# Kernel tuning notes

Measured on AMD Instinct MI355X. Metric: run time of the kernel, lower is better.

## Reference

```python
import jax, jax.numpy as jnp
import numpy as np

BATCH, SEQ, DIM, NH = 4, 2048, 1024, 16
HD = DIM // NH  # 64

def _rope_cos_sin(seq_len, head_dim, dtype=jnp.float32):
    inv_freq = 1.0 / (10000.0 ** (jnp.arange(0, head_dim, 2, dtype=dtype) / head_dim))
    t = jnp.arange(seq_len, dtype=dtype)
    freqs = jnp.outer(t, inv_freq)                # (seq, hd/2)
    emb = jnp.concatenate([freqs, freqs], axis=-1)  # (seq, hd)
    return jnp.cos(emb), jnp.sin(emb)

def _apply_rope(x, cos, sin):
    # x: (b, h, s, d); cos/sin: (s, d)
    d2 = x.shape[-1] // 2
    x1, x2 = x[..., :d2], x[..., d2:]
    c = cos[None, None, :, :d2]
    s = sin[None, None, :, :d2]
    return jnp.concatenate([x1 * c - x2 * s, x1 * s + x2 * c], axis=-1)

def setup_inputs() -> dict:
    key = jax.random.key(0)
    ks = jax.random.split(key, 3)
    x = jax.random.normal(ks[0], (BATCH, SEQ, DIM), dtype=jnp.float32)
    Wqkv = jax.random.normal(ks[1], (DIM, 3 * DIM), dtype=jnp.float32) * (1.0 / np.sqrt(DIM))
    bqkv = jnp.zeros((3 * DIM,), dtype=jnp.float32)
    Wout = jax.random.normal(ks[2], (DIM, DIM), dtype=jnp.float32) * (1.0 / np.sqrt(DIM))
    bout = jnp.zeros((DIM,), dtype=jnp.float32)
    return {"x": x, "Wqkv": Wqkv, "bqkv": bqkv, "Wout": Wout, "bout": bout}

def reference(x, Wqkv, bqkv, Wout, bout):
    b, s, dim = x.shape
    qkv = x @ Wqkv + bqkv                          # (b, s, 3*dim)
    qkv = qkv.reshape(b, s, 3, NH, HD).transpose(2, 0, 3, 1, 4)  # (3, b, h, s, hd)
    q, k, v = qkv[0], qkv[1], qkv[2]
    cos, sin = _rope_cos_sin(s, HD, x.dtype)
    q = _apply_rope(q, cos, sin)
    k = _apply_rope(k, cos, sin)
    scale = HD ** -0.5
    scores = jnp.einsum('bhqd,bhkd->bhqk', q, k) * scale
    attn = jax.nn.softmax(scores, axis=-1)
    attn = jnp.nan_to_num(attn, nan=0.0)
    out = jnp.einsum('bhqk,bhkd->bhqd', attn, v)   # (b, h, s, hd)
    out = out.transpose(0, 2, 1, 3).reshape(b, s, dim)
    return out @ Wout + bout
```

## Files before the change

### kernel.cpp

```cpp
#include <hip/hip_runtime.h>
#include <hip/hip_bf16.h>
#include <stdint.h>

#define DEVI __device__ __forceinline__

typedef __attribute__((ext_vector_type(8))) short bf16x8;
typedef __attribute__((ext_vector_type(4))) float f32x4;

DEVI float bf2f(short u) {
  union { unsigned int i; float f; } v;
  v.i = ((unsigned int)(unsigned short)u) << 16;
  return v.f;
}
DEVI short f2bf(float f) {
  union { float f; unsigned int i; } v; v.f = f;
  unsigned int r = v.i + 0x7FFFu + ((v.i >> 16) & 1u);
  return (short)(r >> 16);
}

DEVI bf16x8 ldsfrag(const short* t, int row, int k0) {
  int slot = k0 >> 3;
  return *(const bf16x8*)(t + row * 64 + ((slot ^ (row & 7)) << 3));
}

DEVI void gload16(const void* g, void* l) {
  __builtin_amdgcn_global_load_lds((const __attribute__((address_space(1))) void*)g,
                                   (__attribute__((address_space(3))) void*)l, 16, 0, 0);
}

__global__ void k_cvt(const float* __restrict__ in, short* __restrict__ out, int n4) {
  int i = blockIdx.x * blockDim.x + threadIdx.x;
  if (i >= n4) return;
  float4 v = ((const float4*)in)[i];
  short4 o;
  o.x = f2bf(v.x); o.y = f2bf(v.y); o.z = f2bf(v.z); o.w = f2bf(v.w);
  ((short4*)out)[i] = o;
}

__global__ void k_transpose_bf16(const float* __restrict__ in, short* __restrict__ outp,
                                 int R, int C) {
  __shared__ float tile[32][33];
  const int c0 = blockIdx.x * 32, r0 = blockIdx.y * 32;
  const int tx = threadIdx.x, ty = threadIdx.y;
  for (int i = ty; i < 32; i += 8) tile[i][tx] = in[(size_t)(r0 + i) * C + c0 + tx];
  __syncthreads();
  for (int i = ty; i < 32; i += 8) outp[(size_t)(c0 + i) * R + r0 + tx] = f2bf(tile[tx][i]);
}

__global__ void k_rope(float* __restrict__ cosT, float* __restrict__ sinT) {
  int idx = blockIdx.x * blockDim.x + threadIdx.x;
  int s = idx >> 5, i = idx & 31;
  float inv = exp2f(-0.41524101186092034f * (float)i);
  float freq = (float)s * inv;
  cosT[idx] = cosf(freq);
  sinT[idx] = sinf(freq);
}

template <int OUTF32>
__global__ __launch_bounds__(256) void k_gemm(const short* __restrict__ A,
                                              const short* __restrict__ BT,
                                              const float* __restrict__ bias,
                                              void* __restrict__ outp,
                                              int M, int N, int K) {
  __shared__ __align__(16) short As[128 * 64];
  __shared__ __align__(16) short Bs[128 * 64];
  const int tid = threadIdx.x;
  const int lane = tid & 63, wid = tid >> 6;
  const int ln = lane & 15, grp = lane >> 4;
  const int wm = wid >> 1, wn = wid & 1;
  const int r0 = blockIdx.y * 128, c0 = blockIdx.x * 128;

  const short* aSrc[4];
  const short* bSrc[4];
  int ldst[4];
#pragma unroll
  for (int j = 0; j < 4; ++j) {
    int chunk = wid * 256 + j * 64 + lane;
    int row = chunk >> 3, gs = (chunk & 7) ^ (row & 7);
    aSrc[j] = A + (size_t)(r0 + row) * K + gs * 8;
    bSrc[j] = BT + (size_t)(c0 + row) * K + gs * 8;
    ldst[j] = (wid * 256 + j * 64) * 8;
  }

  f32x4 acc[4][4];
#pragma unroll
  for (int i = 0; i < 4; ++i)
#pragma unroll
    for (int j = 0; j < 4; ++j) acc[i][j] = (f32x4){0.f, 0.f, 0.f, 0.f};

  const int nkt = K >> 6;
  for (int kt = 0; kt < nkt; ++kt) {
    __syncthreads();
#pragma unroll
    for (int j = 0; j < 4; ++j) {
      gload16(aSrc[j], &As[ldst[j]]);
      gload16(bSrc[j], &Bs[ldst[j]]);
      aSrc[j] += 64;
      bSrc[j] += 64;
    }
    __syncthreads();
#pragma unroll
    for (int ks = 0; ks < 2; ++ks) {
      const int k0 = ks * 32 + grp * 8;
      bf16x8 af[4], bfr[4];
#pragma unroll
      for (int mi = 0; mi < 4; ++mi) af[mi] = ldsfrag(As, wm * 64 + mi * 16 + ln, k0);
#pragma unroll
      for (int ni = 0; ni < 4; ++ni) bfr[ni] = ldsfrag(Bs, wn * 64 + ni * 16 + ln, k0);
#pragma unroll
      for (int mi = 0; mi < 4; ++mi)
#pragma unroll
        for (int ni = 0; ni < 4; ++ni)
          acc[mi][ni] = __builtin_amdgcn_mfma_f32_16x16x32_bf16(af[mi], bfr[ni], acc[mi][ni], 0, 0, 0);
    }
  }
#pragma unroll
  for (int ni = 0; ni < 4; ++ni) {
    const int col = c0 + wn * 64 + ni * 16 + ln;
    const float bv = bias[col];
#pragma unroll
    for (int mi = 0; mi < 4; ++mi) {
#pragma unroll
      for (int r = 0; r < 4; ++r) {
        const int rowg = r0 + wm * 64 + mi * 16 + grp * 4 + r;
        float v = acc[mi][ni][r] + bv;
        if (OUTF32) ((float*)outp)[(size_t)rowg * N + col] = v;
        else        ((short*)outp)[(size_t)rowg * N + col] = f2bf(v);
      }
    }
  }
}

__global__ __launch_bounds__(256) void k_transform(const short* __restrict__ qkv,
                                                   const float* __restrict__ cosT,
                                                   const float* __restrict__ sinT,
                                                   short* __restrict__ qo,
                                                   short* __restrict__ ko,
                                                   short* __restrict__ vp) {
  __shared__ __align__(16) short vs[64 * 72];
  const int st = blockIdx.x, bh = blockIdx.y;
  const int b = bh >> 4, h = bh & 15;
  const int t = threadIdx.x;
  const float QSC = 0.18033688011112042f;
  {
    const int sl = t >> 2, j = t & 3;
    const int s = st * 64 + sl;
    const short* row = qkv + ((size_t)(b * 2048 + s)) * 3072 + h * 64;
    bf16x8 qlo = *(const bf16x8*)(row + j * 8);
    bf16x8 qhi = *(const bf16x8*)(row + 32 + j * 8);
    bf16x8 klo = *(const bf16x8*)(row + 1024 + j * 8);
    bf16x8 khi = *(const bf16x8*)(row + 1056 + j * 8);
    const float* cp = cosT + s * 32 + j * 8;
    const float* sp = sinT + s * 32 + j * 8;
    bf16x8 ql, qh, kl, kh;
#pragma unroll
    for (int e = 0; e < 8; ++e) {
      float c = cp[e], sn = sp[e];
      float a1 = bf2f(qlo[e]), a2 = bf2f(qhi[e]);
      ql[e] = f2bf((a1 * c - a2 * sn) * QSC);
      qh[e] = f2bf((a1 * sn + a2 * c) * QSC);
      float b1 = bf2f(klo[e]), b2 = bf2f(khi[e]);
      kl[e] = f2bf(b1 * c - b2 * sn);
      kh[e] = f2bf(b1 * sn + b2 * c);
    }
    short* qrow = qo + ((size_t)bh * 2048 + s) * 64;
    short* krow = ko + ((size_t)bh * 2048 + s) * 64;
    *(bf16x8*)(qrow + j * 8) = ql;
    *(bf16x8*)(qrow + 32 + j * 8) = qh;
    *(bf16x8*)(krow + j * 8) = kl;
    *(bf16x8*)(krow + 32 + j * 8) = kh;
    bf16x8 v0 = *(const bf16x8*)(row + 2048 + j * 16);
    bf16x8 v1 = *(const bf16x8*)(row + 2048 + j * 16 + 8);
    *(bf16x8*)(&vs[sl * 72 + j * 16]) = v0;
    *(bf16x8*)(&vs[sl * 72 + j * 16 + 8]) = v1;
  }
  __syncthreads();
  {
#pragma unroll
    for (int i = 0; i < 2; ++i) {
      const int cc = t + i * 256;
      const int ks = cc >> 8, mi = (cc >> 6) & 3, grp = (cc >> 4) & 3, ln = cc & 15;
      const int d = mi * 16 + ln;
      bf16x8 o;
#pragma unroll
      for (int e = 0; e < 8; ++e) {
        const int key = 32 * ks + 16 * (e >> 2) + 4 * grp + (e & 3);
        o[e] = vs[key * 72 + d];
      }
      *(bf16x8*)(vp + ((size_t)bh * 32 + st) * 4096 + cc * 8) = o;
    }
  }
}

__global__ __launch_bounds__(256) void k_attn(const short* __restrict__ Q,
                                              const short* __restrict__ Kk,
                                              const short* __restrict__ Vp,
                                              short* __restrict__ out) {
  __shared__ __align__(16) short smem[128 * 64];
  short* Ks = smem;
  const int tid = threadIdx.x;
  const int lane = tid & 63, wid = tid >> 6;
  const int ln = lane & 15, grp = lane >> 4;
  const int qt = blockIdx.x, bh = blockIdx.y;
  const int b = bh >> 4, h = bh & 15;

  bf16x8 qf[2][2];
#pragma unroll
  for (int g = 0; g < 2; ++g)
#pragma unroll
    for (int ks = 0; ks < 2; ++ks)
      qf[g][ks] = *(const bf16x8*)(Q + ((size_t)bh * 2048 + qt * 128 + wid * 32 + g * 16 + ln) * 64
                                   + ks * 32 + grp * 8);

  const short* kSrc0;
  const short* kSrc1;
  int ldst0, ldst1;
  {
    int c0i = wid * 64 + lane;
    int r0i = c0i >> 3, g0i = (c0i & 7) ^ (r0i & 7);
    kSrc0 = Kk + (size_t)bh * 2048 * 64 + (size_t)r0i * 64 + g0i * 8;
    ldst0 = (wid * 64) * 8;
    int c1i = 256 + wid * 64 + lane;
    int r1i = c1i >> 3, g1i = (c1i & 7) ^ (r1i & 7);
    kSrc1 = Kk + (size_t)bh * 2048 * 64 + (size_t)r1i * 64 + g1i * 8;
    ldst1 = (256 + wid * 64) * 8;
  }

  f32x4 acc[2][4];
  f32x4 accl[2];
#pragma unroll
  for (int g = 0; g < 2; ++g) {
    accl[g] = (f32x4){0.f, 0.f, 0.f, 0.f};
#pragma unroll
    for (int i = 0; i < 4; ++i) acc[g][i] = (f32x4){0.f, 0.f, 0.f, 0.f};
  }
  bf16x8 ones;
#pragma unroll
  for (int e = 0; e < 8; ++e) ones[e] = (short)0x3F80;

  union PU { bf16x8 v; unsigned int u[4]; };

  for (int t = 0; t < 32; ++t) {
    const short* vt = Vp + ((size_t)bh * 32 + t) * 4096;
    bf16x8 vf0[4];
#pragma unroll
    for (int mi = 0; mi < 4; ++mi) vf0[mi] = *(const bf16x8*)(vt + mi * 512 + lane * 8);

    __syncthreads();
    gload16(kSrc0, &Ks[ldst0]);
    gload16(kSrc1, &Ks[ldst1]);
    kSrc0 += 4096;
    kSrc1 += 4096;
    __syncthreads();

    f32x4 sf[2][4];
#pragma unroll
    for (int g = 0; g < 2; ++g)
#pragma unroll
      for (int ni = 0; ni < 4; ++ni) sf[g][ni] = (f32x4){0.f, 0.f, 0.f, 0.f};
#pragma unroll
    for (int ks = 0; ks < 2; ++ks) {
      bf16x8 kf[4];
#pragma unroll
      for (int ni = 0; ni < 4; ++ni) kf[ni] = ldsfrag(Ks, ni * 16 + ln, ks * 32 + grp * 8);
      __builtin_amdgcn_s_setprio(1);
#pragma unroll
      for (int g = 0; g < 2; ++g)
#pragma unroll
        for (int ni = 0; ni < 4; ++ni)
          sf[g][ni] = __builtin_amdgcn_mfma_f32_16x16x32_bf16(kf[ni], qf[g][ks], sf[g][ni], 0, 0, 0);
      __builtin_amdgcn_s_setprio(0);
    }

    bf16x8 vf1[4];
#pragma unroll
    for (int mi = 0; mi < 4; ++mi) vf1[mi] = *(const bf16x8*)(vt + 2048 + mi * 512 + lane * 8);

    PU pbf[2][2];
#pragma unroll
    for (int g = 0; g < 2; ++g) {
#pragma unroll
      for (int ni = 0; ni < 4; ++ni) {
        f32x4 s = sf[g][ni];
#pragma unroll
        for (int r = 0; r < 4; ++r) s[r] = __builtin_amdgcn_exp2f(s[r]);
        sf[g][ni] = s;
      }
#pragma unroll
      for (int ks = 0; ks < 2; ++ks)
#pragma unroll
        for (int j = 0; j < 4; ++j) {
          float lo = sf[g][2 * ks + (j >> 1)][(j & 1) * 2];
          float hi = sf[g][2 * ks + (j >> 1)][(j & 1) * 2 + 1];
          unsigned int r;
          asm("v_cvt_pk_bf16_f32 %0, %1, %2" : "=v"(r) : "v"(lo), "v"(hi));
          pbf[g][ks].u[j] = r;
        }
    }

    __builtin_amdgcn_s_setprio(1);
#pragma unroll
    for (int g = 0; g < 2; ++g) {
#pragma unroll
      for (int mi = 0; mi < 4; ++mi)
        acc[g][mi] = __builtin_amdgcn_mfma_f32_16x16x32_bf16(vf0[mi], pbf[g][0].v, acc[g][mi], 0, 0, 0);
      accl[g] = __builtin_amdgcn_mfma_f32_16x16x32_bf16(ones, pbf[g][0].v, accl[g], 0, 0, 0);
    }
#pragma unroll
    for (int g = 0; g < 2; ++g) {
#pragma unroll
      for (int mi = 0; mi < 4; ++mi)
        acc[g][mi] = __builtin_amdgcn_mfma_f32_16x16x32_bf16(vf1[mi], pbf[g][1].v, acc[g][mi], 0, 0, 0);
      accl[g] = __builtin_amdgcn_mfma_f32_16x16x32_bf16(ones, pbf[g][1].v, accl[g], 0, 0, 0);
    }
    __builtin_amdgcn_s_setprio(0);
  }

  __syncthreads();
#pragma unroll
  for (int g = 0; g < 2; ++g) {
    const float inv = 1.0f / accl[g][0];
    const int q = wid * 32 + g * 16 + ln;
#pragma unroll
    for (int mi = 0; mi < 4; ++mi) {
      short4 p;
      p.x = f2bf(acc[g][mi][0] * inv);
      p.y = f2bf(acc[g][mi][1] * inv);
      p.z = f2bf(acc[g][mi][2] * inv);
      p.w = f2bf(acc[g][mi][3] * inv);
      int slot = mi * 2 + (grp >> 1);
      *(short4*)(&smem[q * 64 + ((slot ^ (q & 7)) << 3) + (grp & 1) * 4]) = p;
    }
  }
  __syncthreads();
  {
    const int row = tid >> 1, half = tid & 1;
#pragma unroll
    for (int j = 0; j < 4; ++j) {
      int c = half * 4 + j;
      int4 v = *(const int4*)(&smem[row * 64 + ((c ^ (row & 7)) << 3)]);
      *(int4*)(out + ((size_t)b * 2048 + qt * 128 + row) * 1024 + h * 64 + c * 8) = v;
    }
  }
}

extern "C" void kernel_launch(void* const* d_in, const int* in_sizes, int n_in,
                              void* d_out, int out_size, void* d_ws, size_t ws_size,
                              hipStream_t stream) {
  const float* x    = (const float*)d_in[0];
  const float* Wqkv = (const float*)d_in[1];
  const float* bqkv = (const float*)d_in[2];
  const float* Wout = (const float*)d_in[3];
  const float* bout = (const float*)d_in[4];
  float* out = (float*)d_out;

  char* p = (char*)d_ws;
  short* xb    = (short*)p; p += (size_t)8192 * 1024 * 2;
  short* wqkvT = (short*)p; p += (size_t)3072 * 1024 * 2;
  short* woutT = (short*)p; p += (size_t)1024 * 1024 * 2;
  float* cosT  = (float*)p; p += (size_t)2048 * 32 * 4;
  float* sinT  = (float*)p; p += (size_t)2048 * 32 * 4;
  short* qkvb  = (short*)p; p += (size_t)8192 * 3072 * 2;
  short* qb    = (short*)p; p += (size_t)64 * 2048 * 64 * 2;
  short* kb    = (short*)p; p += (size_t)64 * 2048 * 64 * 2;
  short* vpb   = (short*)p; p += (size_t)64 * 2048 * 64 * 2;
  short* ao    = (short*)p; p += (size_t)8192 * 1024 * 2;

  k_cvt<<<8192 * 1024 / 4 / 256, 256, 0, stream>>>(x, xb, 8192 * 1024 / 4);
  k_transpose_bf16<<<dim3(3072 / 32, 1024 / 32), dim3(32, 8), 0, stream>>>(Wqkv, wqkvT, 1024, 3072);
  k_transpose_bf16<<<dim3(1024 / 32, 1024 / 32), dim3(32, 8), 0, stream>>>(Wout, woutT, 1024, 1024);
  k_rope<<<2048 * 32 / 256, 256, 0, stream>>>(cosT, sinT);
  k_gemm<0><<<dim3(3072 / 128, 8192 / 128), 256, 0, stream>>>(xb, wqkvT, bqkv, (void*)qkvb,
                                                              8192, 3072, 1024);
  k_transform<<<dim3(32, 64), 256, 0, stream>>>(qkvb, cosT, sinT, qb, kb, vpb);
  k_attn<<<dim3(16, 64), 256, 0, stream>>>(qb, kb, vpb, ao);
  k_gemm<1><<<dim3(1024 / 128, 8192 / 128), 256, 0, stream>>>(ao, woutT, bout, (void*)out,
                                                              8192, 1024, 1024);
}
```

Baseline: 226.6 us.

## Double-buffer K and V tiles in LDS with async prefetch in attention

The attention loop now keeps two LDS buffers holding both the K and V tiles. The next tile is prefetched with async global-to-LDS loads while the current one is computed, and each iteration ends with a single barrier instead of two. V is now read from LDS rather than loaded straight from global memory into registers. The aim is to hide global load latency behind the MFMA work, at the cost of twice the LDS per block, which may lower occupancy.

Result: faster. 217.9 us (-3.8%).

```diff
diff --git a/kernel.cpp b/kernel.cpp
--- a/kernel.cpp
+++ b/kernel.cpp
@@ -196,8 +196,7 @@
                                               const short* __restrict__ Kk,
                                               const short* __restrict__ Vp,
                                               short* __restrict__ out) {
-  __shared__ __align__(16) short smem[128 * 64];
-  short* Ks = smem;
+  __shared__ __align__(16) short smem[2 * 8192];
   const int tid = threadIdx.x;
   const int lane = tid & 63, wid = tid >> 6;
   const int ln = lane & 15, grp = lane >> 4;
@@ -214,16 +213,23 @@
 
   const short* kSrc0;
   const short* kSrc1;
-  int ldst0, ldst1;
+  const short* vSrc0;
+  const short* vSrc1;
+  int ldk0, ldk1, ldv0, ldv1;
   {
     int c0i = wid * 64 + lane;
     int r0i = c0i >> 3, g0i = (c0i & 7) ^ (r0i & 7);
     kSrc0 = Kk + (size_t)bh * 2048 * 64 + (size_t)r0i * 64 + g0i * 8;
-    ldst0 = (wid * 64) * 8;
+    ldk0 = wid * 512;
     int c1i = 256 + wid * 64 + lane;
     int r1i = c1i >> 3, g1i = (c1i & 7) ^ (r1i & 7);
     kSrc1 = Kk + (size_t)bh * 2048 * 64 + (size_t)r1i * 64 + g1i * 8;
-    ldst1 = (256 + wid * 64) * 8;
+    ldk1 = 2048 + wid * 512;
+    const short* vt = Vp + (size_t)bh * 32 * 4096;
+    vSrc0 = vt + (size_t)c0i * 8;
+    ldv0 = 4096 + wid * 512;
+    vSrc1 = vt + (size_t)c1i * 8;
+    ldv1 = 4096 + 2048 + wid * 512;
   }
 
   f32x4 acc[2][4];
@@ -240,18 +246,25 @@
 
   union PU { bf16x8 v; unsigned int u[4]; };
 
+  gload16(kSrc0, &smem[ldk0]);
+  gload16(kSrc1, &smem[ldk1]);
+  gload16(vSrc0, &smem[ldv0]);
+  gload16(vSrc1, &smem[ldv1]);
+  kSrc0 += 4096; kSrc1 += 4096; vSrc0 += 4096; vSrc1 += 4096;
+  __syncthreads();
+
+  int cur = 0;
   for (int t = 0; t < 32; ++t) {
-    const short* vt = Vp + ((size_t)bh * 32 + t) * 4096;
-    bf16x8 vf0[4];
-#pragma unroll
-    for (int mi = 0; mi < 4; ++mi) vf0[mi] = *(const bf16x8*)(vt + mi * 512 + lane * 8);
-
-    __syncthreads();
-    gload16(kSrc0, &Ks[ldst0]);
-    gload16(kSrc1, &Ks[ldst1]);
-    kSrc0 += 4096;
-    kSrc1 += 4096;
-    __syncthreads();
+    if (t < 31) {
+      const int bo = (cur ^ 1) * 8192;
+      gload16(kSrc0, &smem[bo + ldk0]);
+      gload16(kSrc1, &smem[bo + ldk1]);
+      gload16(vSrc0, &smem[bo + ldv0]);
+      gload16(vSrc1, &smem[bo + ldv1]);
+      kSrc0 += 4096; kSrc1 += 4096; vSrc0 += 4096; vSrc1 += 4096;
+    }
+    const short* Kb = smem + cur * 8192;
+    const short* Vb = Kb + 4096;
 
     f32x4 sf[2][4];
 #pragma unroll
@@ -262,7 +275,7 @@
     for (int ks = 0; ks < 2; ++ks) {
       bf16x8 kf[4];
 #pragma unroll
-      for (int ni = 0; ni < 4; ++ni) kf[ni] = ldsfrag(Ks, ni * 16 + ln, ks * 32 + grp * 8);
+      for (int ni = 0; ni < 4; ++ni) kf[ni] = ldsfrag(Kb, ni * 16 + ln, ks * 32 + grp * 8);
       __builtin_amdgcn_s_setprio(1);
 #pragma unroll
       for (int g = 0; g < 2; ++g)
@@ -271,10 +284,6 @@
           sf[g][ni] = __builtin_amdgcn_mfma_f32_16x16x32_bf16(kf[ni], qf[g][ks], sf[g][ni], 0, 0, 0);
       __builtin_amdgcn_s_setprio(0);
     }
-
-    bf16x8 vf1[4];
-#pragma unroll
-    for (int mi = 0; mi < 4; ++mi) vf1[mi] = *(const bf16x8*)(vt + 2048 + mi * 512 + lane * 8);
 
     PU pbf[2][2];
 #pragma unroll
@@ -298,25 +307,27 @@
         }
     }
 
-    __builtin_amdgcn_s_setprio(1);
-#pragma unroll
-    for (int g = 0; g < 2; ++g) {
+#pragma unroll
+    for (int ks = 0; ks < 2; ++ks) {
+      bf16x8 vf[4];
 #pragma unroll
       for (int mi = 0; mi < 4; ++mi)
-        acc[g][mi] = __builtin_amdgcn_mfma_f32_16x16x32_bf16(vf0[mi], pbf[g][0].v, acc[g][mi], 0, 0, 0);
-      accl[g] = __builtin_amdgcn_mfma_f32_16x16x32_bf16(ones, pbf[g][0].v, accl[g], 0, 0, 0);
-    }
-#pragma unroll
-    for (int g = 0; g < 2; ++g) {
-#pragma unroll
-      for (int mi = 0; mi < 4; ++mi)
-        acc[g][mi] = __builtin_amdgcn_mfma_f32_16x16x32_bf16(vf1[mi], pbf[g][1].v, acc[g][mi], 0, 0, 0);
-      accl[g] = __builtin_amdgcn_mfma_f32_16x16x32_bf16(ones, pbf[g][1].v, accl[g], 0, 0, 0);
-    }
-    __builtin_amdgcn_s_setprio(0);
-  }
-
-  __syncthreads();
+        vf[mi] = *(const bf16x8*)(Vb + (ks * 256 + mi * 64 + lane) * 8);
+      __builtin_amdgcn_s_setprio(1);
+#pragma unroll
+      for (int g = 0; g < 2; ++g) {
+#pragma unroll
+        for (int mi = 0; mi < 4; ++mi)
+          acc[g][mi] = __builtin_amdgcn_mfma_f32_16x16x32_bf16(vf[mi], pbf[g][ks].v, acc[g][mi], 0, 0, 0);
+        accl[g] = __builtin_amdgcn_mfma_f32_16x16x32_bf16(ones, pbf[g][ks].v, accl[g], 0, 0, 0);
+      }
+      __builtin_amdgcn_s_setprio(0);
+    }
+
+    __syncthreads();
+    cur ^= 1;
+  }
+
 #pragma unroll
   for (int g = 0; g < 2; ++g) {
     const float inv = 1.0f / accl[g][0];
```
